# Optimization experiments

Measured on AMD Instinct MI355X. Metric: run time of the kernel, lower is better.

Reference implementation:

```python
import jax, jax.numpy as jnp
import numpy as np

L, D = 2048, 1024
D_INNER = 2 * D          # expand=2
D_STATE = 16
D_CONV = 4
DT_RANK = D // 16        # ceil(1024/16) = 64
HID = 4 * D
EPS = 1e-5


def _layernorm(x, g, b):
    mu = jnp.mean(x, axis=-1, keepdims=True)
    var = jnp.mean(jnp.square(x - mu), axis=-1, keepdims=True)
    return (x - mu) * jax.lax.rsqrt(var + EPS) * g + b


def setup_inputs() -> dict:
    key = jax.random.key(0)
    ks = jax.random.split(key, 12)
    f = lambda k, sh, s=0.02: (jax.random.normal(k, sh, jnp.float32) * s)
    return {
        "x": jax.random.normal(ks[0], (L, D), jnp.float32),
        "ln1_g": jnp.ones((D,), jnp.float32),
        "ln1_b": jnp.zeros((D,), jnp.float32),
        "ln2_g": jnp.ones((D,), jnp.float32),
        "ln2_b": jnp.zeros((D,), jnp.float32),
        "in_proj_w": f(ks[1], (2 * D_INNER, D)),
        "conv_w": f(ks[2], (D_INNER, D_CONV), 0.1),
        "conv_b": jnp.zeros((D_INNER,), jnp.float32),
        "x_proj_w": f(ks[3], (DT_RANK + 2 * D_STATE, D_INNER)),
        "dt_proj_w": f(ks[4], (D_INNER, DT_RANK), 0.1),
        "dt_proj_b": f(ks[5], (D_INNER,), 0.1),
        "A_log": jnp.log(jnp.broadcast_to(
            jnp.arange(1, D_STATE + 1, dtype=jnp.float32), (D_INNER, D_STATE))),
        "D_param": jnp.ones((D_INNER,), jnp.float32),
        "out_proj_w": f(ks[6], (D, D_INNER)),
        "ffn_w1": f(ks[7], (HID, D)),
        "ffn_b1": jnp.zeros((HID,), jnp.float32),
        "ffn_w2": f(ks[8], (D, HID)),
        "ffn_b2": jnp.zeros((D,), jnp.float32),
    }


def _mamba(x, in_proj_w, conv_w, conv_b, x_proj_w, dt_proj_w, dt_proj_b,
           A_log, D_param, out_proj_w):
    # x: (L, D)
    xz = x @ in_proj_w.T                    # (L, 2*d_inner)
    xm, z = xz[:, :D_INNER], xz[:, D_INNER:]
    # causal depthwise conv1d, kernel d_conv, output length L
    xp = jnp.pad(xm, ((D_CONV - 1, 0), (0, 0)))
    xc = conv_b
    for k in range(D_CONV):                 # 4 taps, fixed small loop
        xc = xc + xp[k:k + L] * conv_w[None, :, k]
    xc = jax.nn.silu(xc)                    # (L, d_inner)
    proj = xc @ x_proj_w.T                  # (L, dt_rank + 2*d_state)
    dt = proj[:, :DT_RANK]
    B = proj[:, DT_RANK:DT_RANK + D_STATE]  # (L, d_state)
    C = proj[:, DT_RANK + D_STATE:]         # (L, d_state)
    delta = jax.nn.softplus(dt @ dt_proj_w.T + dt_proj_b)  # (L, d_inner)
    A = -jnp.exp(A_log)                     # (d_inner, d_state)
    dA = jnp.exp(delta[:, :, None] * A[None])               # (L, d_inner, d_state)
    dBx = delta[:, :, None] * B[:, None, :] * xc[:, :, None]

    def step(h, inp):
        dA_t, dBx_t, C_t = inp
        h = h * dA_t + dBx_t                # (d_inner, d_state)
        y = jnp.einsum('ds,s->d', h, C_t)
        return h, y

    h0 = jnp.zeros((D_INNER, D_STATE), x.dtype)
    _, ys = jax.lax.scan(step, h0, (dA, dBx, C))            # ys: (L, d_inner)
    y = ys + xc * D_param
    y = y * jax.nn.silu(z)
    return y @ out_proj_w.T                 # (L, D)


def reference(x, ln1_g, ln1_b, ln2_g, ln2_b, in_proj_w, conv_w, conv_b,
              x_proj_w, dt_proj_w, dt_proj_b, A_log, D_param, out_proj_w,
              ffn_w1, ffn_b1, ffn_w2, ffn_b2):
    residual = x
    h = _layernorm(x, ln1_g, ln1_b)
    h = _mamba(h, in_proj_w, conv_w, conv_b, x_proj_w, dt_proj_w, dt_proj_b,
               A_log, D_param, out_proj_w)
    h = h + residual
    # FFN has an internal residual around the normed input, plus outer residual
    n = _layernorm(h, ln2_g, ln2_b)
    f = n + (jax.nn.relu(n @ ffn_w1.T + ffn_b1) @ ffn_w2.T + ffn_b2)
    return h + f
```

## Files before the change

kernel.cpp:

```cpp
#include <hip/hip_runtime.h>
#include <hip/hip_bf16.h>
#include <math.h>

#define L_SEQ 2048
#define DMODEL 1024
#define DINNER 2048
#define DSTATE 16
#define DTRANK 64
#define NHID 4096
#define NC 64
#define LC 32

typedef __bf16 bf16_t;
typedef __bf16 bf16x4 __attribute__((ext_vector_type(4)));
typedef __bf16 bf16x8 __attribute__((ext_vector_type(8)));
typedef float f32x4 __attribute__((ext_vector_type(4)));

#define WAIT_VM0 0x0F70
#define WAIT_VM4 0x0F74
#define WAIT_VM8 0x0F78

__device__ __forceinline__ void async_cp16(const bf16_t* g, bf16_t* l) {
    __builtin_amdgcn_global_load_lds(
        (const __attribute__((address_space(1))) void*)g,
        (__attribute__((address_space(3))) void*)l, 16, 0, 0);
}

template <int EPI, int OUTBF16, int SWZ>
__global__ __launch_bounds__(256) void gemm_async(
    const bf16_t* __restrict__ A, int lda,
    const bf16_t* __restrict__ W, int ldw,
    void* __restrict__ Cv, int ldc,
    int N, int Kslice, long cstride,
    const float* __restrict__ bias)
{
    __shared__ bf16_t As[4 * 4096];
    __shared__ bf16_t Ws[4 * 4096];

    const int tid  = threadIdx.x;
    const int lane = tid & 63;
    const int w    = tid >> 6;

    int bx = blockIdx.x, by = blockIdx.y;
    if (SWZ == 1) {
        int lid = by * 32 + bx;
        int r = lid & 7, i = lid >> 3;
        bx = (r & 3) * 8 + (i & 7);
        by = (r >> 2) * 8 + (i >> 3);
    }
    const int m0   = by * 128;
    const int n0   = bx * 128;
    const int kz   = blockIdx.z;
    const int k0   = kz * Kslice;

    const int p   = lane & 3;
    const int r0  = 2 * w * 16 + (lane >> 2);
    const int r1  = r0 + 16;
    const int dc0 = (p - ((r0 >> 1) & 3)) & 3;
    const int dc1 = (p - ((r1 >> 1) & 3)) & 3;

    const bf16_t* gA0 = A + (size_t)(m0 + r0) * lda + k0 + dc0 * 8;
    const bf16_t* gA1 = A + (size_t)(m0 + r1) * lda + k0 + dc1 * 8;
    int gn0 = n0 + r0; if (gn0 > N - 1) gn0 = N - 1;
    int gn1 = n0 + r1; if (gn1 > N - 1) gn1 = N - 1;
    const bf16_t* gW0 = W + (size_t)gn0 * ldw + k0 + dc0 * 8;
    const bf16_t* gW1 = W + (size_t)gn1 * ldw + k0 + dc1 * 8;

    const int lo0 = (2 * w) * 512;
    const int lo1 = lo0 + 512;

    const int wr   = w >> 1;
    const int wc   = w & 1;
    const int quad = lane >> 4;
    const int lr   = lane & 15;
    int offA[4], offW[4];
    #pragma unroll
    for (int i = 0; i < 4; ++i) {
        int ra = wr * 64 + i * 16 + lr;
        offA[i] = ra * 32 + (((quad + ((ra >> 1) & 3)) & 3) * 8);
        int rb = wc * 64 + i * 16 + lr;
        offW[i] = rb * 32 + (((quad + ((rb >> 1) & 3)) & 3) * 8);
    }

    const int niter = Kslice >> 5;

    #pragma unroll
    for (int j = 0; j < 3; ++j) {
        if (j < niter) {
            int sb = j * 4096;
            async_cp16(gA0, &As[sb + lo0]);
            async_cp16(gA1, &As[sb + lo1]);
            async_cp16(gW0, &Ws[sb + lo0]);
            async_cp16(gW1, &Ws[sb + lo1]);
            gA0 += 32; gA1 += 32; gW0 += 32; gW1 += 32;
        }
    }

    f32x4 acc[4][4] = {};
    for (int it = 0; it < niter; ++it) {
        if (it + 3 <= niter)      __builtin_amdgcn_s_waitcnt(WAIT_VM8);
        else if (it + 2 <= niter) __builtin_amdgcn_s_waitcnt(WAIT_VM4);
        else                      __builtin_amdgcn_s_waitcnt(WAIT_VM0);
        __builtin_amdgcn_s_barrier();
        asm volatile("" ::: "memory");

        if (it + 3 < niter) {
            int sb = ((it + 3) & 3) * 4096;
            async_cp16(gA0, &As[sb + lo0]);
            async_cp16(gA1, &As[sb + lo1]);
            async_cp16(gW0, &Ws[sb + lo0]);
            async_cp16(gW1, &Ws[sb + lo1]);
            gA0 += 32; gA1 += 32; gW0 += 32; gW1 += 32;
        }

        const int cb = (it & 3) * 4096;
        bf16x8 af[4], bw[4];
        #pragma unroll
        for (int i = 0; i < 4; ++i) af[i] = *(const bf16x8*)&As[cb + offA[i]];
        #pragma unroll
        for (int j = 0; j < 4; ++j) bw[j] = *(const bf16x8*)&Ws[cb + offW[j]];
        #pragma unroll
        for (int i = 0; i < 4; ++i)
            #pragma unroll
            for (int j = 0; j < 4; ++j)
                acc[i][j] = __builtin_amdgcn_mfma_f32_16x16x32_bf16(af[i], bw[j], acc[i][j], 0, 0, 0);
    }

    float*  Cf = (float*)Cv + (size_t)kz * cstride;
    bf16_t* Cb = (bf16_t*)Cv + (size_t)kz * cstride;
    #pragma unroll
    for (int i = 0; i < 4; ++i) {
        int row0 = m0 + wr * 64 + i * 16 + quad * 4;
        #pragma unroll
        for (int j = 0; j < 4; ++j) {
            int col = n0 + wc * 64 + j * 16 + lr;
            if (col < N) {
                float bv = (EPI == 2 || EPI == 3) ? bias[col] : 0.f;
                #pragma unroll
                for (int r = 0; r < 4; ++r) {
                    float v = acc[i][j][r];
                    if (EPI == 2) v = fmaxf(v + bv, 0.f);
                    else if (EPI == 3) {
                        float t = v + bv;
                        v = fmaxf(t, 0.f) + log1pf(__expf(-fabsf(t)));
                    }
                    size_t o = (size_t)(row0 + r) * ldc + col;
                    if (OUTBF16) Cb[o] = (bf16_t)v;
                    else         Cf[o] = v;
                }
            }
        }
    }
}

__global__ __launch_bounds__(256) void cvt_ln1(
    const float* __restrict__ s0, const float* __restrict__ s1,
    const float* __restrict__ s2, const float* __restrict__ s3,
    const float* __restrict__ s4, const float* __restrict__ s5,
    bf16_t* __restrict__ dst,
    const float* __restrict__ x, const float* __restrict__ g,
    const float* __restrict__ b, bf16_t* __restrict__ outb)
{
    if (blockIdx.x < 14656) {
        int e = (blockIdx.x * 256 + threadIdx.x) * 4;
        const float* src; int local;
        if      (e < 4194304)  { src = s0; local = e; }
        else if (e < 4390912)  { src = s1; local = e - 4194304; }
        else if (e < 4521984)  { src = s2; local = e - 4390912; }
        else if (e < 6619136)  { src = s3; local = e - 4521984; }
        else if (e < 10813440) { src = s4; local = e - 6619136; }
        else                   { src = s5; local = e - 10813440; }
        float4 v = *(const float4*)(src + local);
        bf16x4 o;
        o[0] = (bf16_t)v.x; o[1] = (bf16_t)v.y; o[2] = (bf16_t)v.z; o[3] = (bf16_t)v.w;
        *(bf16x4*)(dst + e) = o;
        return;
    }
    const int row = blockIdx.x - 14656;
    const float* xr = x + (size_t)row * DMODEL;
    float v[4];
    float s = 0.f, sq = 0.f;
    #pragma unroll
    for (int i = 0; i < 4; ++i) {
        v[i] = xr[threadIdx.x + i * 256];
        s += v[i]; sq += v[i] * v[i];
    }
    #pragma unroll
    for (int off = 32; off > 0; off >>= 1) {
        s += __shfl_xor(s, off); sq += __shfl_xor(sq, off);
    }
    __shared__ float rs_[4], rq_[4];
    int w = threadIdx.x >> 6;
    if ((threadIdx.x & 63) == 0) { rs_[w] = s; rq_[w] = sq; }
    __syncthreads();
    s  = rs_[0] + rs_[1] + rs_[2] + rs_[3];
    sq = rq_[0] + rq_[1] + rq_[2] + rq_[3];
    float mu  = s * (1.f / DMODEL);
    float var = sq * (1.f / DMODEL) - mu * mu;
    float rsd = rsqrtf(var + 1e-5f);
    #pragma unroll
    for (int i = 0; i < 4; ++i) {
        int col = threadIdx.x + i * 256;
        outb[(size_t)row * DMODEL + col] = (bf16_t)((v[i] - mu) * rsd * g[col] + b[col]);
    }
}

__global__ __launch_bounds__(256) void conv_silu(
    const bf16_t* __restrict__ xz, const float* __restrict__ cw,
    const float* __restrict__ cb, bf16_t* __restrict__ xc)
{
    int gid = blockIdx.x * 256 + threadIdx.x;
    int c = gid & (DINNER - 1);
    int t = gid >> 11;
    float acc = cb[c];
    #pragma unroll
    for (int k = 0; k < 4; ++k) {
        int tt = t + k - 3;
        if (tt >= 0) acc += (float)xz[(size_t)tt * (2 * DINNER) + c] * cw[c * 4 + k];
    }
    float sig = 1.f / (1.f + __expf(-acc));
    xc[gid] = (bf16_t)(acc * sig);
}

__global__ __launch_bounds__(256) void scan_pass1(
    const bf16_t* __restrict__ delta, const bf16_t* __restrict__ xc,
    const float* __restrict__ proj, const float* __restrict__ A_log,
    float* __restrict__ carryH, float* __restrict__ sumd)
{
    const int c = blockIdx.x;
    const int d = blockIdx.y * 256 + threadIdx.x;
    const int t0 = c * LC;

    __shared__ float Bs[LC][DSTATE];
    for (int i = threadIdx.x; i < LC * DSTATE; i += 256) {
        int tt = i >> 4, s = i & 15;
        Bs[tt][s] = proj[(size_t)(t0 + tt) * 96 + DTRANK + s];
    }
    __syncthreads();

    float a[DSTATE], h[DSTATE];
    #pragma unroll
    for (int s = 0; s < DSTATE; ++s) {
        a[s] = -__expf(A_log[d * DSTATE + s]);
        h[s] = 0.f;
    }
    float sd = 0.f;
    for (int i = 0; i < LC; ++i) {
        int t = t0 + i;
        float dl = (float)delta[(size_t)t * DINNER + d];
        float x  = (float)xc[(size_t)t * DINNER + d];
        sd += dl;
        float dx = dl * x;
        #pragma unroll
        for (int s = 0; s < DSTATE; ++s)
            h[s] = h[s] * __expf(dl * a[s]) + dx * Bs[i][s];
    }
    #pragma unroll
    for (int s = 0; s < DSTATE; ++s)
        carryH[((size_t)c * DINNER + d) * DSTATE + s] = h[s];
    sumd[c * DINNER + d] = sd;
}

__global__ __launch_bounds__(256) void scan_pass2(
    const float* __restrict__ A_log, const float* __restrict__ carryH,
    const float* __restrict__ sumd, float* __restrict__ hinit)
{
    int idx = blockIdx.x * 256 + threadIdx.x;
    int d = idx >> 4;
    float a = -__expf(A_log[idx]);
    float hc = 0.f;
    for (int c0 = 0; c0 < NC; c0 += 8) {
        float H[8], P[8];
        #pragma unroll
        for (int j = 0; j < 8; ++j) {
            H[j] = carryH[(size_t)(c0 + j) * (DINNER * DSTATE) + idx];
            P[j] = __expf(a * sumd[(c0 + j) * DINNER + d]);
        }
        #pragma unroll
        for (int j = 0; j < 8; ++j) {
            hinit[(size_t)(c0 + j) * (DINNER * DSTATE) + idx] = hc;
            hc = H[j] + P[j] * hc;
        }
    }
}

__global__ __launch_bounds__(256) void scan_pass3(
    const bf16_t* __restrict__ delta, const bf16_t* __restrict__ xc,
    const float* __restrict__ proj, const float* __restrict__ A_log,
    const float* __restrict__ hinit, const float* __restrict__ Dp,
    const bf16_t* __restrict__ xz, bf16_t* __restrict__ yact)
{
    const int c = blockIdx.x;
    const int d = blockIdx.y * 256 + threadIdx.x;
    const int t0 = c * LC;

    __shared__ float Bs[LC][DSTATE], Cs[LC][DSTATE];
    for (int i = threadIdx.x; i < LC * DSTATE; i += 256) {
        int tt = i >> 4, s = i & 15;
        size_t base = (size_t)(t0 + tt) * 96;
        Bs[tt][s] = proj[base + DTRANK + s];
        Cs[tt][s] = proj[base + DTRANK + DSTATE + s];
    }
    __syncthreads();

    float a[DSTATE], h[DSTATE];
    #pragma unroll
    for (int s = 0; s < DSTATE; ++s) {
        a[s] = -__expf(A_log[d * DSTATE + s]);
        h[s] = hinit[(size_t)c * (DINNER * DSTATE) + d * DSTATE + s];
    }
    float DD = Dp[d];
    for (int i = 0; i < LC; ++i) {
        int t = t0 + i;
        float dl = (float)delta[(size_t)t * DINNER + d];
        float x  = (float)xc[(size_t)t * DINNER + d];
        float dx = dl * x;
        float y = 0.f;
        #pragma unroll
        for (int s = 0; s < DSTATE; ++s) {
            h[s] = h[s] * __expf(dl * a[s]) + dx * Bs[i][s];
            y += h[s] * Cs[i][s];
        }
        float yv = y + x * DD;
        float z = (float)xz[(size_t)t * (2 * DINNER) + DINNER + d];
        float sil = z / (1.f + __expf(-z));
        yact[(size_t)t * DINNER + d] = (bf16_t)(yv * sil);
    }
}

__global__ __launch_bounds__(256) void reduce4(
    const float* __restrict__ part, float* __restrict__ proj,
    bf16_t* __restrict__ projdt)
{
    int i = blockIdx.x * 256 + threadIdx.x;
    float v = 0.f;
    #pragma unroll
    for (int s = 0; s < 16; ++s) v += part[(size_t)s * 196608 + i];
    proj[i] = v;
    int row = i / 96;
    int col = i - row * 96;
    if (col < DTRANK) projdt[row * DTRANK + col] = (bf16_t)v;
}

__global__ __launch_bounds__(256) void red9_ln2(
    const bf16_t* __restrict__ part, const float* __restrict__ x,
    const float* __restrict__ g, const float* __restrict__ b,
    float* __restrict__ hres, float* __restrict__ nbuf,
    bf16_t* __restrict__ nbufb)
{
    const int row = blockIdx.x;
    const size_t base = (size_t)row * DMODEL;
    float v[4];
    float s = 0.f, sq = 0.f;
    #pragma unroll
    for (int i = 0; i < 4; ++i) {
        int col = threadIdx.x + i * 256;
        float acc = x[base + col];
        #pragma unroll
        for (int sl = 0; sl < 4; ++sl)
            acc += (float)part[(size_t)sl * 2097152 + base + col];
        hres[base + col] = acc;
        v[i] = acc; s += acc; sq += acc * acc;
    }
    #pragma unroll
    for (int off = 32; off > 0; off >>= 1) {
        s += __shfl_xor(s, off); sq += __shfl_xor(sq, off);
    }
    __shared__ float rs_[4], rq_[4];
    int w = threadIdx.x >> 6;
    if ((threadIdx.x & 63) == 0) { rs_[w] = s; rq_[w] = sq; }
    __syncthreads();
    s  = rs_[0] + rs_[1] + rs_[2] + rs_[3];
    sq = rq_[0] + rq_[1] + rq_[2] + rq_[3];
    float mu  = s * (1.f / DMODEL);
    float var = sq * (1.f / DMODEL) - mu * mu;
    float rsd = rsqrtf(var + 1e-5f);
    #pragma unroll
    for (int i = 0; i < 4; ++i) {
        int col = threadIdx.x + i * 256;
        float o = (v[i] - mu) * rsd * g[col] + b[col];
        nbuf[base + col] = o;
        nbufb[base + col] = (bf16_t)o;
    }
}

__global__ __launch_bounds__(256) void reduce12(
    const bf16_t* __restrict__ part, const float* __restrict__ b2,
    const float* __restrict__ hres, const float* __restrict__ nbuf,
    float* __restrict__ out)
{
    int i = (blockIdx.x * 256 + threadIdx.x) * 4;
    float4 bb = *(const float4*)(b2 + (i & (DMODEL - 1)));
    float4 h  = *(const float4*)(hres + i);
    float4 n  = *(const float4*)(nbuf + i);
    float s0 = bb.x + h.x + n.x, s1 = bb.y + h.y + n.y;
    float s2 = bb.z + h.z + n.z, s3 = bb.w + h.w + n.w;
    #pragma unroll
    for (int sl = 0; sl < 4; ++sl) {
        bf16x4 v = *(const bf16x4*)(part + (size_t)sl * 2097152 + i);
        s0 += (float)v[0]; s1 += (float)v[1]; s2 += (float)v[2]; s3 += (float)v[3];
    }
    *(float4*)(out + i) = make_float4(s0, s1, s2, s3);
}

extern "C" void kernel_launch(void* const* d_in, const int* in_sizes, int n_in,
                              void* d_out, int out_size, void* d_ws, size_t ws_size,
                              hipStream_t stream)
{
    const float* x        = (const float*)d_in[0];
    const float* ln1_g    = (const float*)d_in[1];
    const float* ln1_b    = (const float*)d_in[2];
    const float* ln2_g    = (const float*)d_in[3];
    const float* ln2_b    = (const float*)d_in[4];
    const float* in_proj  = (const float*)d_in[5];
    const float* conv_w   = (const float*)d_in[6];
    const float* conv_b   = (const float*)d_in[7];
    const float* x_proj   = (const float*)d_in[8];
    const float* dt_proj  = (const float*)d_in[9];
    const float* dt_b     = (const float*)d_in[10];
    const float* A_log    = (const float*)d_in[11];
    const float* D_param  = (const float*)d_in[12];
    const float* out_proj = (const float*)d_in[13];
    const float* ffn_w1   = (const float*)d_in[14];
    const float* ffn_b1   = (const float*)d_in[15];
    const float* ffn_w2   = (const float*)d_in[16];
    const float* ffn_b2   = (const float*)d_in[17];
    float* out = (float*)d_out;

    char* base = (char*)d_ws;
    bf16_t* Wb     = (bf16_t*)(base);
    bf16_t* w_inp  = Wb;
    bf16_t* w_xp   = Wb + 4194304;
    bf16_t* w_dtp  = Wb + 4390912;
    bf16_t* w_outp = Wb + 4521984;
    bf16_t* w_f1   = Wb + 6619136;
    bf16_t* w_f2   = Wb + 10813440;

    bf16_t* h1b    = (bf16_t*)(base + 30015488);
    float*  proj   = (float*)(base + 30015488);
    bf16_t* projdt = (bf16_t*)(base + 30015488 + 786432);
    bf16_t* xz     = (bf16_t*)(base + 34209792);
    bf16_t* ffnh   = xz;
    bf16_t* xc     = (bf16_t*)(base + 50987008);
    float*  part   = (float*)(base + 59375616);
    bf16_t* delta  = (bf16_t*)part;
    bf16_t* partb  = (bf16_t*)part;
    float*  carry  = (float*)(base + 76152832);
    bf16_t* nbufb  = (bf16_t*)carry;
    float*  sumd   = (float*)(base + 84541440);
    float*  hinit  = (float*)(base + 85065728);
    float*  nbuf   = hinit;
    bf16_t* yact   = (bf16_t*)(base + 93454336);
    float*  hres   = (float*)(base + 101842944);

    cvt_ln1<<<14656 + 2048, 256, 0, stream>>>(in_proj, x_proj, dt_proj, out_proj,
                                              ffn_w1, ffn_w2, Wb,
                                              x, ln1_g, ln1_b, h1b);
    gemm_async<0, 1, 1><<<dim3(32, 16, 1), 256, 0, stream>>>(
        h1b, DMODEL, w_inp, DMODEL, xz, 4096, 4096, 1024, 0, nullptr);
    conv_silu<<<(L_SEQ * DINNER) / 256, 256, 0, stream>>>(xz, conv_w, conv_b, xc);
    gemm_async<0, 0, 0><<<dim3(1, 16, 16), 256, 0, stream>>>(
        xc, DINNER, w_xp, DINNER, part, 96, 96, 128, 196608L, nullptr);
    reduce4<<<768, 256, 0, stream>>>(part, proj, projdt);
    gemm_async<3, 1, 0><<<dim3(16, 16, 1), 256, 0, stream>>>(
        projdt, DTRANK, w_dtp, DTRANK, delta, DINNER, DINNER, DTRANK, 0, dt_b);
    scan_pass1<<<dim3(NC, DINNER / 256), 256, 0, stream>>>(delta, xc, proj, A_log, carry, sumd);
    scan_pass2<<<(DINNER * DSTATE) / 256, 256, 0, stream>>>(A_log, carry, sumd, hinit);
    scan_pass3<<<dim3(NC, DINNER / 256), 256, 0, stream>>>(delta, xc, proj, A_log, hinit,
                                                           D_param, xz, yact);
    gemm_async<0, 1, 0><<<dim3(8, 16, 4), 256, 0, stream>>>(
        yact, DINNER, w_outp, DINNER, partb, DMODEL, DMODEL, 512, 2097152L, nullptr);
    red9_ln2<<<L_SEQ, 256, 0, stream>>>(partb, x, ln2_g, ln2_b, hres, nbuf, nbufb);
    gemm_async<2, 1, 1><<<dim3(32, 16, 1), 256, 0, stream>>>(
        nbufb, DMODEL, w_f1, DMODEL, ffnh, NHID, NHID, 1024, 0, ffn_b1);
    gemm_async<0, 1, 0><<<dim3(8, 16, 4), 256, 0, stream>>>(
        ffnh, NHID, w_f2, NHID, partb, DMODEL, DMODEL, 1024, 2097152L, nullptr);
    reduce12<<<2048, 256, 0, stream>>>(partb, ffn_b2, hres, nbuf, out);
}
```

Measured before the change: 371.6 us.

## Add 256x128-tile 512-thread GEMM kernel for the four large projections

Adds a gemm_big kernel with 256x128 output tiles, 8 waves per block and double-buffered async LDS loads, and routes the in_proj, out_proj, FFN1 and FFN2 GEMMs through it. The taller tile halves the number of blocks and re-reads each weight tile across twice as many rows, cutting global and LDS traffic per MFMA. It also uses new block-index swizzles for L2 locality, including across the split-K slices. In exchange each block holds more LDS, and a shallower 2-stage pipeline (versus 4 buffers before) may expose more load latency.

```diff
diff --git a/kernel.cpp b/kernel.cpp
--- a/kernel.cpp
+++ b/kernel.cpp
@@ -26,7 +26,122 @@
         (__attribute__((address_space(3))) void*)l, 16, 0, 0);
 }
 
-template <int EPI, int OUTBF16, int SWZ>
+template <int EPI, int SPLIT>
+__global__ __launch_bounds__(512, 4) void gemm_big(
+    const bf16_t* __restrict__ A, int lda,
+    const bf16_t* __restrict__ W, int ldw,
+    bf16_t* __restrict__ C, int ldc,
+    int Kslice, long cstride,
+    const float* __restrict__ bias)
+{
+    __shared__ bf16_t As[2 * 8192];
+    __shared__ bf16_t Ws[2 * 4096];
+
+    const int tid  = threadIdx.x;
+    const int lane = tid & 63;
+    const int w    = tid >> 6;
+
+    int my, mx, kz;
+    if (SPLIT == 0) {
+        int lid = blockIdx.y * 32 + blockIdx.x;
+        int r = lid & 7, i = lid >> 3;
+        my = (r >> 2) * 4 + (i & 3);
+        mx = (r & 3) * 8 + (i >> 2);
+        kz = 0;
+    } else {
+        int id = (blockIdx.z * 8 + blockIdx.y) * 8 + blockIdx.x;
+        int r = id & 7, i = id >> 3;
+        kz = r >> 1;
+        my = i & 7;
+        mx = (r & 1) * 4 + (i >> 3);
+    }
+    const int m0 = my * 256;
+    const int n0 = mx * 128;
+    const int k0 = kz * Kslice;
+
+    const int p    = lane & 3;
+    const int rA0  = 2 * w * 16 + (lane >> 2);
+    const int rA1  = rA0 + 16;
+    const int rW   = w * 16 + (lane >> 2);
+    const int dcA0 = (p - ((rA0 >> 1) & 3)) & 3;
+    const int dcA1 = (p - ((rA1 >> 1) & 3)) & 3;
+    const int dcW  = (p - ((rW  >> 1) & 3)) & 3;
+
+    const bf16_t* gA0 = A + (size_t)(m0 + rA0) * lda + k0 + dcA0 * 8;
+    const bf16_t* gA1 = A + (size_t)(m0 + rA1) * lda + k0 + dcA1 * 8;
+    const bf16_t* gW  = W + (size_t)(n0 + rW) * ldw + k0 + dcW * 8;
+    const int aLo0 = (2 * w) * 512;
+    const int aLo1 = aLo0 + 512;
+    const int wLo  = w * 512;
+
+    const int wr   = w >> 1;
+    const int wc   = w & 1;
+    const int quad = lane >> 4;
+    const int lr   = lane & 15;
+    int offA[4], offW[4];
+    #pragma unroll
+    for (int i = 0; i < 4; ++i) {
+        int ra = wr * 64 + i * 16 + lr;
+        offA[i] = ra * 32 + (((quad + ((ra >> 1) & 3)) & 3) * 8);
+        int rb = wc * 64 + i * 16 + lr;
+        offW[i] = rb * 32 + (((quad + ((rb >> 1) & 3)) & 3) * 8);
+    }
+
+    const int niter = Kslice >> 5;
+
+    async_cp16(gA0, &As[aLo0]);
+    async_cp16(gA1, &As[aLo1]);
+    async_cp16(gW,  &Ws[wLo]);
+    gA0 += 32; gA1 += 32; gW += 32;
+
+    f32x4 acc[4][4] = {};
+    for (int it = 0; it < niter; ++it) {
+        __builtin_amdgcn_s_waitcnt(WAIT_VM0);
+        __builtin_amdgcn_s_barrier();
+        asm volatile("" ::: "memory");
+
+        if (it + 1 < niter) {
+            int sa = ((it + 1) & 1) * 8192;
+            int sw = ((it + 1) & 1) * 4096;
+            async_cp16(gA0, &As[sa + aLo0]);
+            async_cp16(gA1, &As[sa + aLo1]);
+            async_cp16(gW,  &Ws[sw + wLo]);
+            gA0 += 32; gA1 += 32; gW += 32;
+        }
+
+        const int ca = (it & 1) * 8192;
+        const int cw = (it & 1) * 4096;
+        bf16x8 af[4], bw[4];
+        #pragma unroll
+        for (int i = 0; i < 4; ++i) af[i] = *(const bf16x8*)&As[ca + offA[i]];
+        #pragma unroll
+        for (int j = 0; j < 4; ++j) bw[j] = *(const bf16x8*)&Ws[cw + offW[j]];
+        #pragma unroll
+        for (int i = 0; i < 4; ++i)
+            #pragma unroll
+            for (int j = 0; j < 4; ++j)
+                acc[i][j] = __builtin_amdgcn_mfma_f32_16x16x32_bf16(af[i], bw[j], acc[i][j], 0, 0, 0);
+    }
+
+    bf16_t* Cb = C + (size_t)kz * cstride;
+    #pragma unroll
+    for (int i = 0; i < 4; ++i) {
+        int row0 = m0 + wr * 64 + i * 16 + quad * 4;
+        #pragma unroll
+        for (int j = 0; j < 4; ++j) {
+            int col = n0 + wc * 64 + j * 16 + lr;
+            float bv = (EPI == 2) ? bias[col] : 0.f;
+            #pragma unroll
+            for (int r = 0; r < 4; ++r) {
+                float v = acc[i][j][r];
+                if (EPI == 2) v = fmaxf(v + bv, 0.f);
+                Cb[(size_t)(row0 + r) * ldc + col] = (bf16_t)v;
+            }
+        }
+    }
+}
+
+template <int EPI, int OUTBF16>
 __global__ __launch_bounds__(256) void gemm_async(
     const bf16_t* __restrict__ A, int lda,
     const bf16_t* __restrict__ W, int ldw,
@@ -40,16 +155,8 @@
     const int tid  = threadIdx.x;
     const int lane = tid & 63;
     const int w    = tid >> 6;
-
-    int bx = blockIdx.x, by = blockIdx.y;
-    if (SWZ == 1) {
-        int lid = by * 32 + bx;
-        int r = lid & 7, i = lid >> 3;
-        bx = (r & 3) * 8 + (i & 7);
-        by = (r >> 2) * 8 + (i >> 3);
-    }
-    const int m0   = by * 128;
-    const int n0   = bx * 128;
+    const int m0   = blockIdx.y * 128;
+    const int n0   = blockIdx.x * 128;
     const int kz   = blockIdx.z;
     const int k0   = kz * Kslice;
 
@@ -135,12 +242,11 @@
         for (int j = 0; j < 4; ++j) {
             int col = n0 + wc * 64 + j * 16 + lr;
             if (col < N) {
-                float bv = (EPI == 2 || EPI == 3) ? bias[col] : 0.f;
+                float bv = (EPI == 3) ? bias[col] : 0.f;
                 #pragma unroll
                 for (int r = 0; r < 4; ++r) {
                     float v = acc[i][j][r];
-                    if (EPI == 2) v = fmaxf(v + bv, 0.f);
-                    else if (EPI == 3) {
+                    if (EPI == 3) {
                         float t = v + bv;
                         v = fmaxf(t, 0.f) + log1pf(__expf(-fabsf(t)));
                     }
@@ -456,24 +562,24 @@
     cvt_ln1<<<14656 + 2048, 256, 0, stream>>>(in_proj, x_proj, dt_proj, out_proj,
                                               ffn_w1, ffn_w2, Wb,
                                               x, ln1_g, ln1_b, h1b);
-    gemm_async<0, 1, 1><<<dim3(32, 16, 1), 256, 0, stream>>>(
-        h1b, DMODEL, w_inp, DMODEL, xz, 4096, 4096, 1024, 0, nullptr);
+    gemm_big<0, 0><<<dim3(32, 8), 512, 0, stream>>>(
+        h1b, DMODEL, w_inp, DMODEL, xz, 4096, 1024, 0, nullptr);
     conv_silu<<<(L_SEQ * DINNER) / 256, 256, 0, stream>>>(xz, conv_w, conv_b, xc);
-    gemm_async<0, 0, 0><<<dim3(1, 16, 16), 256, 0, stream>>>(
+    gemm_async<0, 0><<<dim3(1, 16, 16), 256, 0, stream>>>(
         xc, DINNER, w_xp, DINNER, part, 96, 96, 128, 196608L, nullptr);
     reduce4<<<768, 256, 0, stream>>>(part, proj, projdt);
-    gemm_async<3, 1, 0><<<dim3(16, 16, 1), 256, 0, stream>>>(
+    gemm_async<3, 1><<<dim3(16, 16, 1), 256, 0, stream>>>(
         projdt, DTRANK, w_dtp, DTRANK, delta, DINNER, DINNER, DTRANK, 0, dt_b);
     scan_pass1<<<dim3(NC, DINNER / 256), 256, 0, stream>>>(delta, xc, proj, A_log, carry, sumd);
     scan_pass2<<<(DINNER * DSTATE) / 256, 256, 0, stream>>>(A_log, carry, sumd, hinit);
     scan_pass3<<<dim3(NC, DINNER / 256), 256, 0, stream>>>(delta, xc, proj, A_log, hinit,
                                                            D_param, xz, yact);
-    gemm_async<0, 1, 0><<<dim3(8, 16, 4), 256, 0, stream>>>(
-        yact, DINNER, w_outp, DINNER, partb, DMODEL, DMODEL, 512, 2097152L, nullptr);
+    gemm_big<0, 1><<<dim3(8, 8, 4), 512, 0, stream>>>(
+        yact, DINNER, w_outp, DINNER, partb, DMODEL, 512, 2097152L, nullptr);
     red9_ln2<<<L_SEQ, 256, 0, stream>>>(partb, x, ln2_g, ln2_b, hres, nbuf, nbufb);
-    gemm_async<2, 1, 1><<<dim3(32, 16, 1), 256, 0, stream>>>(
-        nbufb, DMODEL, w_f1, DMODEL, ffnh, NHID, NHID, 1024, 0, ffn_b1);
-    gemm_async<0, 1, 0><<<dim3(8, 16, 4), 256, 0, stream>>>(
-        ffnh, NHID, w_f2, NHID, partb, DMODEL, DMODEL, 1024, 2097152L, nullptr);
+    gemm_big<2, 0><<<dim3(32, 8), 512, 0, stream>>>(
+        nbufb, DMODEL, w_f1, DMODEL, ffnh, NHID, 1024, 0, ffn_b1);
+    gemm_big<0, 1><<<dim3(8, 8, 4), 512, 0, stream>>>(
+        ffnh, NHID, w_f2, NHID, partb, DMODEL, 1024, 2097152L, nullptr);
     reduce12<<<2048, 256, 0, stream>>>(partb, ffn_b2, hres, nbuf, out);
 }
```

Measured after the change: 417.3 us. 12.3% more time.
